# Kernel tuning notes

Measured on AMD Instinct MI355X. Metric: run time of the kernel, lower is better.

The kernel has to match this reference:

```python
import jax, jax.numpy as jnp
import numpy as np

N = 50000   # num_nodes
D = 128     # h_dim
R = 32      # num_rels * 2 (forward + inverse relations)
B = 8       # num_bases
E = 600000  # num_edges


def setup_inputs() -> dict:
    key = jax.random.key(0)
    ks = jax.random.split(key, 14)
    s = 1.0 / np.sqrt(D)
    return {
        "h_ids": jnp.arange(N, dtype=jnp.int32),
        "src": jax.random.randint(ks[0], (E,), 0, N),
        "dst": jax.random.randint(ks[1], (E,), 0, N),
        "etype": jax.random.randint(ks[2], (E,), 0, R),
        "norm": jax.random.uniform(ks[3], (E, 1), dtype=jnp.float32),
        "embedding": jax.random.normal(ks[4], (N, D), dtype=jnp.float32) * 0.05,
        "w_comp1": jax.random.normal(ks[5], (R, B), dtype=jnp.float32) * (1.0 / np.sqrt(B)),
        "bases1": jax.random.normal(ks[6], (B, D, D), dtype=jnp.float32) * s,
        "loop_w1": jax.random.normal(ks[7], (D, D), dtype=jnp.float32) * s,
        "bias1": jnp.zeros((D,), dtype=jnp.float32),
        "w_comp2": jax.random.normal(ks[8], (R, B), dtype=jnp.float32) * (1.0 / np.sqrt(B)),
        "bases2": jax.random.normal(ks[9], (B, D, D), dtype=jnp.float32) * s,
        "loop_w2": jax.random.normal(ks[10], (D, D), dtype=jnp.float32) * s,
        "bias2": jnp.zeros((D,), dtype=jnp.float32),
    }


def _rel_graph_conv(h, src, dst, etype, norm, w_comp, bases, loop_w, bias, act):
    # basis decomposition: W[r] = sum_b w_comp[r,b] * bases[b]
    W = jnp.einsum('rb,bio->rio', w_comp, bases)          # [R, D, D]
    # transform every node by every relation weight (dense GEMM)
    all_t = jnp.einsum('ni,rio->nro', h, W)               # [N, R, D]
    # per-edge gather of relation-specific transformed source features
    msg = all_t[src, etype] * norm                        # [E, D]
    # scatter-aggregate messages at destination nodes
    agg = jax.ops.segment_sum(msg, dst, num_segments=h.shape[0])  # [N, D]
    out = agg + h @ loop_w + bias                         # self-loop + bias
    return act(out) if act is not None else out


def reference(h_ids, src, dst, etype, norm, embedding,
              w_comp1, bases1, loop_w1, bias1,
              w_comp2, bases2, loop_w2, bias2):
    # EmbeddingLayer
    h = embedding[h_ids]                                  # [N, D]
    # hidden layer 0: relu activation (idx < num_hidden_layers-1)
    h = _rel_graph_conv(h, src, dst, etype, norm, w_comp1, bases1, loop_w1, bias1, jax.nn.relu)
    # hidden layer 1: no activation (last layer)
    h = _rel_graph_conv(h, src, dst, etype, norm, w_comp2, bases2, loop_w2, bias2, None)
    return h
```

## Files before the change

### kernel.cpp

```cpp
#include <hip/hip_runtime.h>

#define DD 128
#define NB 8
#define KTOT 1152

typedef unsigned int uint_t;
typedef __attribute__((ext_vector_type(8))) _Float16 half8v;
typedef __attribute__((ext_vector_type(2))) _Float16 half2v;
typedef __attribute__((ext_vector_type(4))) float f32x4;

static __device__ __forceinline__ void gld_lds16(const _Float16* g, _Float16* l)
{
  __builtin_amdgcn_global_load_lds(
      (const __attribute__((address_space(1))) void*)g,
      (__attribute__((address_space(3))) void*)l, 16, 0, 0);
}

static __device__ __forceinline__ half2v bc_h2(uint_t u)
{
  union { uint_t u; half2v h; } c; c.u = u; return c.h;
}

static __device__ __forceinline__ float fdot2(uint_t a, uint_t b, float acc)
{
#if __has_builtin(__builtin_amdgcn_fdot2)
  return __builtin_amdgcn_fdot2(bc_h2(a), bc_h2(b), acc, false);
#else
  half2v x = bc_h2(a), y = bc_h2(b);
  return acc + (float)x[0] * (float)y[0] + (float)x[1] * (float)y[1];
#endif
}

__global__ __launch_bounds__(256) void k_prep_w(
    const float* __restrict__ bases1, const float* __restrict__ loopw1,
    const float* __restrict__ bases2, const float* __restrict__ loopw2,
    _Float16* __restrict__ WcA)
{
  int i = blockIdx.x * 256 + threadIdx.x;
  if (i >= 2 * 36 * DD * 32) return;
  int layer = i / (36 * DD * 32);
  int rem   = i % (36 * DD * 32);
  int ks    = rem / (DD * 32);
  int rem2  = rem % (DD * 32);
  int feat  = rem2 / 32;
  int j     = rem2 % 32;
  int k     = ks * 32 + j;
  const float* basesL = layer ? bases2 : bases1;
  const float* loopwL = layer ? loopw2 : loopw1;
  float v;
  if (k < 1024) {
    int kk = k >> 3, b = k & 7;
    v = basesL[((size_t)b * DD + kk) * DD + feat];
  } else {
    v = loopwL[(size_t)(k - 1024) * DD + feat];
  }
  WcA[i] = (_Float16)v;
}

__global__ __launch_bounds__(256) void k_cast(
    const float* __restrict__ h, const int* __restrict__ ids,
    _Float16* __restrict__ hf, int N)
{
  int i = blockIdx.x * 256 + threadIdx.x;
  if (i >= N * (DD / 8)) return;
  int n  = i / (DD / 8);
  int k8 = (i % (DD / 8)) * 8;
  int row = ids ? ids[n] : n;
  const float* hp = h + (size_t)row * DD + k8;
  float4 v0 = *(const float4*)hp;
  float4 v1 = *(const float4*)(hp + 4);
  union { _Float16 e[8]; uint4 q; } p;
  p.e[0]=(_Float16)v0.x; p.e[1]=(_Float16)v0.y; p.e[2]=(_Float16)v0.z; p.e[3]=(_Float16)v0.w;
  p.e[4]=(_Float16)v1.x; p.e[5]=(_Float16)v1.y; p.e[6]=(_Float16)v1.z; p.e[7]=(_Float16)v1.w;
  *(uint4*)&hf[(size_t)n * DD + k8] = p.q;
}

__global__ __launch_bounds__(256) void k_zero(int* __restrict__ p, int n)
{
  int i = blockIdx.x * 256 + threadIdx.x;
  if (i < n) p[i] = 0;
}

__global__ __launch_bounds__(256) void k_hist(
    const int* __restrict__ dst, int* __restrict__ cnt,
    int* __restrict__ slotin, int E)
{
  int e = blockIdx.x * 256 + threadIdx.x;
  if (e < E) slotin[e] = atomicAdd(&cnt[dst[e]], 1);
}

__global__ __launch_bounds__(256) void k_bsum(
    const int* __restrict__ cnt, int* __restrict__ bsum, int N)
{
  __shared__ int s[256];
  int i = blockIdx.x * 256 + threadIdx.x;
  s[threadIdx.x] = (i < N) ? ((cnt[i] + 1) & ~1) : 0;
  __syncthreads();
  for (int off = 128; off > 0; off >>= 1) {
    if (threadIdx.x < off) s[threadIdx.x] += s[threadIdx.x + off];
    __syncthreads();
  }
  if (threadIdx.x == 0) bsum[blockIdx.x] = s[0];
}

__global__ __launch_bounds__(256) void k_scanb(
    const int* __restrict__ bsum, int* __restrict__ boff, int nb)
{
  __shared__ int s[256];
  int t = threadIdx.x;
  int own = (t < nb) ? bsum[t] : 0;
  s[t] = own;
  __syncthreads();
  for (int off = 1; off < 256; off <<= 1) {
    int v = (t >= off) ? s[t - off] : 0;
    __syncthreads();
    s[t] += v;
    __syncthreads();
  }
  if (t < nb) boff[t] = s[t] - own;
}

__global__ __launch_bounds__(256) void k_scan3(
    const int* __restrict__ cnt, const int* __restrict__ boff,
    int* __restrict__ row_start, int* __restrict__ psrc, int N)
{
  __shared__ int s[256];
  int t = threadIdx.x;
  int i = blockIdx.x * 256 + t;
  int c = (i < N) ? cnt[i] : 0;
  int v = (c + 1) & ~1;
  s[t] = v;
  __syncthreads();
  for (int off = 1; off < 256; off <<= 1) {
    int u = (t >= off) ? s[t - off] : 0;
    __syncthreads();
    s[t] += u;
    __syncthreads();
  }
  if (i < N) {
    int rs = boff[blockIdx.x] + s[t] - v;
    row_start[i] = rs;
    if (c & 1) psrc[rs + c] = 0;
  }
}

__global__ __launch_bounds__(256) void k_place(
    const int* __restrict__ dst, const int* __restrict__ src,
    const int* __restrict__ etype, const float* __restrict__ norm,
    const int* __restrict__ row_start, const int* __restrict__ slotin,
    int* __restrict__ psrc, int2* __restrict__ en, int E)
{
  int e = blockIdx.x * 256 + threadIdx.x;
  if (e < E) {
    int slot = row_start[dst[e]] + slotin[e];
    psrc[slot] = src[e];
    en[slot] = make_int2(etype[e], __float_as_int(norm[e]));
  }
}

__global__ __launch_bounds__(256) void k_payload_pair(
    const int2* __restrict__ en,
    const float* __restrict__ wcomp1, const float* __restrict__ wcomp2,
    _Float16* __restrict__ c1, _Float16* __restrict__ c2, int npair)
{
  int i = blockIdx.x * 256 + threadIdx.x;
  if (i >= npair) return;
  int2 e0 = en[2 * i], e1 = en[2 * i + 1];
  float n0 = __int_as_float(e0.y), n1 = __int_as_float(e1.y);
  const float* w10 = wcomp1 + e0.x * NB;
  const float* w11 = wcomp1 + e1.x * NB;
  const float* w20 = wcomp2 + e0.x * NB;
  const float* w21 = wcomp2 + e1.x * NB;

  union { _Float16 h[16]; uint4 q[2]; } p;
  #pragma unroll
  for (int b = 0; b < NB; b++) {
    p.h[b * 2]     = (_Float16)(w10[b] * n0);
    p.h[b * 2 + 1] = (_Float16)(w11[b] * n1);
  }
  *(uint4*)&c1[(size_t)i * 16]     = p.q[0];
  *(uint4*)&c1[(size_t)i * 16 + 8] = p.q[1];
  #pragma unroll
  for (int b = 0; b < NB; b++) {
    p.h[b * 2]     = (_Float16)(w20[b] * n0);
    p.h[b * 2 + 1] = (_Float16)(w21[b] * n1);
  }
  *(uint4*)&c2[(size_t)i * 16]     = p.q[0];
  *(uint4*)&c2[(size_t)i * 16 + 8] = p.q[1];
}

__global__ __launch_bounds__(256) void k_agg(
    const int* __restrict__ rowst, const int* __restrict__ cnt,
    const int* __restrict__ psrc, const _Float16* __restrict__ cpair,
    const _Float16* __restrict__ hf,
    _Float16* __restrict__ agg, int N)
{
  int v = blockIdx.x * 4 + (threadIdx.x >> 6);
  if (v >= N) return;
  int lane = threadIdx.x & 63;
  const uint_t* hf32 = (const uint_t*)hf;
  const int beg = rowst[v];
  const int npairs = (cnt[v] + 1) >> 1;
  const uint_t* cp = (const uint_t*)cpair + (size_t)(beg >> 1) * 8;
  const int* ps = psrc + beg;

  float ax[NB] = {}, ay[NB] = {};
  int i = 0;
  for (; i + 4 <= npairs; i += 4) {
    uint_t u[8], lo[4], hi[4];
    #pragma unroll
    for (int q = 0; q < 8; q++)
      u[q] = hf32[(size_t)ps[2*i + q] * 64 + lane];
    #pragma unroll
    for (int q = 0; q < 4; q++) {
      lo[q] = __builtin_amdgcn_perm(u[2*q], u[2*q+1], 0x01000504);
      hi[q] = __builtin_amdgcn_perm(u[2*q], u[2*q+1], 0x03020706);
    }
    #pragma unroll
    for (int b = 0; b < NB; b++) {
      #pragma unroll
      for (int q = 0; q < 4; q++) {
        uint_t cc = cp[(size_t)(i + q) * 8 + b];
        ax[b] = fdot2(cc, lo[q], ax[b]);
        ay[b] = fdot2(cc, hi[q], ay[b]);
      }
    }
  }
  for (; i + 2 <= npairs; i += 2) {
    uint_t u0 = hf32[(size_t)ps[2*i + 0] * 64 + lane];
    uint_t u1 = hf32[(size_t)ps[2*i + 1] * 64 + lane];
    uint_t u2 = hf32[(size_t)ps[2*i + 2] * 64 + lane];
    uint_t u3 = hf32[(size_t)ps[2*i + 3] * 64 + lane];
    uint_t lo01 = __builtin_amdgcn_perm(u0, u1, 0x01000504);
    uint_t hi01 = __builtin_amdgcn_perm(u0, u1, 0x03020706);
    uint_t lo23 = __builtin_amdgcn_perm(u2, u3, 0x01000504);
    uint_t hi23 = __builtin_amdgcn_perm(u2, u3, 0x03020706);
    #pragma unroll
    for (int b = 0; b < NB; b++) {
      uint_t ca = cp[(size_t)i * 8 + b];
      uint_t cb = cp[(size_t)(i + 1) * 8 + b];
      ax[b] = fdot2(ca, lo01, ax[b]);
      ay[b] = fdot2(ca, hi01, ay[b]);
      ax[b] = fdot2(cb, lo23, ax[b]);
      ay[b] = fdot2(cb, hi23, ay[b]);
    }
  }
  if (i < npairs) {
    uint_t u0 = hf32[(size_t)ps[2*i + 0] * 64 + lane];
    uint_t u1 = hf32[(size_t)ps[2*i + 1] * 64 + lane];
    uint_t lo01 = __builtin_amdgcn_perm(u0, u1, 0x01000504);
    uint_t hi01 = __builtin_amdgcn_perm(u0, u1, 0x03020706);
    #pragma unroll
    for (int b = 0; b < NB; b++) {
      uint_t ca = cp[(size_t)i * 8 + b];
      ax[b] = fdot2(ca, lo01, ax[b]);
      ay[b] = fdot2(ca, hi01, ay[b]);
    }
  }

  union { _Float16 e[8]; uint4 q; } p0, p1;
  #pragma unroll
  for (int b = 0; b < NB; b++) { p0.e[b] = (_Float16)ax[b]; p1.e[b] = (_Float16)ay[b]; }
  uint4* dstp = (uint4*)&agg[(size_t)v * 1024 + lane * 16];
  dstp[0] = p0.q;
  dstp[1] = p1.q;
}

template <int LAYER>
__global__ __launch_bounds__(256) void k_mm(
    const _Float16* __restrict__ agg,
    const _Float16* __restrict__ hf,
    const _Float16* __restrict__ WcA,
    const float* __restrict__ bias,
    float* __restrict__ outf, _Float16* __restrict__ outh, int N)
{
  __shared__ _Float16 sB[2][4096];

  const int n0   = blockIdx.x * 64;
  const int wv   = threadIdx.x >> 6;
  const int lane = threadIdx.x & 63;
  const int l15  = lane & 15, l4 = lane >> 4;

  int nodeL = n0 + lane; if (nodeL >= N) nodeL = N - 1;

  f32x4 acc[2][4];
  #pragma unroll
  for (int a = 0; a < 2; a++)
    #pragma unroll
    for (int b = 0; b < 4; b++) acc[a][b] = (f32x4)0.f;

  const int fbase = wv * 32 + l15;
  const int koff  = l4 * 8;

  auto STAGE = [&](int buf, int t) {
    const _Float16 *g0, *g1;
    if (t < 16) {
      g0 = &agg[(size_t)nodeL * 1024 + (2 * t)     * 32 + wv * 8];
      g1 = &agg[(size_t)nodeL * 1024 + (2 * t + 1) * 32 + wv * 8];
    } else {
      g0 = &hf[(size_t)nodeL * DD + (2 * t - 32) * 32 + wv * 8];
      g1 = &hf[(size_t)nodeL * DD + (2 * t - 31) * 32 + wv * 8];
    }
    gld_lds16(g0, &sB[buf][ wv      * 512]);
    gld_lds16(g1, &sB[buf][(wv + 4) * 512]);
  };

  auto COMPUTE = [&](int buf, int t) {
    #pragma unroll
    for (int sub = 0; sub < 2; sub++) {
      const int ks = 2 * t + sub;
      half8v af[2], bfr[4];
      #pragma unroll
      for (int mf = 0; mf < 2; mf++)
        af[mf] = *(const half8v*)&WcA[((size_t)ks * DD + fbase + mf * 16) * 32 + koff];
      #pragma unroll
      for (int nf = 0; nf < 4; nf++)
        bfr[nf] = *(const half8v*)&sB[buf][(l4 + sub * 4) * 512 + (nf * 16 + l15) * 8];
      #pragma unroll
      for (int mf = 0; mf < 2; mf++)
        #pragma unroll
        for (int nf = 0; nf < 4; nf++)
          acc[mf][nf] = __builtin_amdgcn_mfma_f32_16x16x32_f16(af[mf], bfr[nf], acc[mf][nf], 0, 0, 0);
    }
  };

  STAGE(0, 0);
  __syncthreads();
  int cur = 0;
  for (int t = 0; t < 17; t++) {
    STAGE(cur ^ 1, t + 1);
    COMPUTE(cur, t);
    __syncthreads();
    cur ^= 1;
  }
  COMPUTE(cur, 17);

  #pragma unroll
  for (int mf = 0; mf < 2; mf++)
    #pragma unroll
    for (int nf = 0; nf < 4; nf++) {
      int n = n0 + nf * 16 + l15;
      if (n >= N) continue;
      int feat = wv * 32 + mf * 16 + l4 * 4;
      if (LAYER == 1) {
        union { _Float16 e[4]; uint2 q; } p;
        #pragma unroll
        for (int r = 0; r < 4; r++)
          p.e[r] = (_Float16)fmaxf(acc[mf][nf][r] + bias[feat + r], 0.f);
        *(uint2*)&outh[(size_t)n * DD + feat] = p.q;
      } else {
        float4 o;
        o.x = acc[mf][nf][0] + bias[feat + 0];
        o.y = acc[mf][nf][1] + bias[feat + 1];
        o.z = acc[mf][nf][2] + bias[feat + 2];
        o.w = acc[mf][nf][3] + bias[feat + 3];
        *(float4*)&outf[(size_t)n * DD + feat] = o;
      }
    }
}

extern "C" void kernel_launch(void* const* d_in, const int* in_sizes, int n_in,
                              void* d_out, int out_size, void* d_ws, size_t ws_size,
                              hipStream_t stream)
{
  const int*   h_ids     = (const int*)d_in[0];
  const int*   src       = (const int*)d_in[1];
  const int*   dst       = (const int*)d_in[2];
  const int*   etype     = (const int*)d_in[3];
  const float* norm      = (const float*)d_in[4];
  const float* embedding = (const float*)d_in[5];
  const float* w_comp1   = (const float*)d_in[6];
  const float* bases1    = (const float*)d_in[7];
  const float* loop_w1   = (const float*)d_in[8];
  const float* bias1     = (const float*)d_in[9];
  const float* w_comp2   = (const float*)d_in[10];
  const float* bases2    = (const float*)d_in[11];
  const float* loop_w2   = (const float*)d_in[12];
  const float* bias2     = (const float*)d_in[13];

  const int N = in_sizes[0];
  const int E = in_sizes[1];
  const int S = (E + N) & ~1;
  const int NPAIR = S >> 1;
  const int NBLK = (N + 255) / 256;

  char* base = (char*)d_ws;
  size_t off = 0;
  auto alloc = [&](size_t bytes) -> char* {
    char* p = base + off;
    off += (bytes + 255) & ~(size_t)255;
    return p;
  };
  _Float16* agg  = (_Float16*)alloc((size_t)N * 1024 * 2);
  _Float16* hfp  = (_Float16*)alloc((size_t)N * DD * 2);
  _Float16* h1h  = (_Float16*)alloc((size_t)N * DD * 2);
  _Float16* WcA  = (_Float16*)alloc((size_t)2 * 36 * DD * 32 * 2);
  int*      cnt    = (int*)   alloc((size_t)N * 4);
  int2*     en     = (int2*)  alloc((size_t)S * 8);
  int*      rowst  = (int*)   alloc((size_t)N * 4);
  int*      bsum   = (int*)   alloc(256 * 4);
  int*      boff   = (int*)   alloc(256 * 4);
  int*      slotin = (int*)   alloc((size_t)E * 4);
  int*      psrc   = (int*)   alloc((size_t)S * 4);
  _Float16* c1     = (_Float16*)alloc((size_t)S * 8 * 2);
  _Float16* c2     = (_Float16*)alloc((size_t)S * 8 * 2);
  float*    out    = (float*)d_out;

  int zn = (int)(((char*)(en + S) - (char*)cnt) / 4);
  k_zero <<<(zn + 255) / 256, 256, 0, stream>>>(cnt, zn);
  k_hist <<<(E + 255) / 256, 256, 0, stream>>>(dst, cnt, slotin, E);
  k_bsum <<<NBLK, 256, 0, stream>>>(cnt, bsum, N);
  k_scanb<<<1, 256, 0, stream>>>(bsum, boff, NBLK);
  k_scan3<<<NBLK, 256, 0, stream>>>(cnt, boff, rowst, psrc, N);
  k_place<<<(E + 255) / 256, 256, 0, stream>>>(dst, src, etype, norm,
                                               rowst, slotin, psrc, en, E);
  k_payload_pair<<<(NPAIR + 255) / 256, 256, 0, stream>>>(
      en, w_comp1, w_comp2, c1, c2, NPAIR);

  k_prep_w<<<(2 * 36 * DD * 32 + 255) / 256, 256, 0, stream>>>(bases1, loop_w1, bases2, loop_w2, WcA);

  dim3 gmm((N + 63) / 64);
  int gagg = (N + 3) / 4;

  k_cast<<<(N * (DD / 8) + 255) / 256, 256, 0, stream>>>(embedding, h_ids, hfp, N);
  k_agg<<<gagg, 256, 0, stream>>>(rowst, cnt, psrc, c1, hfp, agg, N);
  k_mm<1><<<gmm, 256, 0, stream>>>(agg, hfp, WcA, bias1, nullptr, h1h, N);

  k_agg<<<gagg, 256, 0, stream>>>(rowst, cnt, psrc, c2, h1h, agg, N);
  k_mm<2><<<gmm, 256, 0, stream>>>(agg, h1h, WcA + (size_t)36 * DD * 32, bias2, out, nullptr, N);
}
```

Measured before the change: 255.7 us.

## Split k_mm across 8 waves and pack edge records into int4

The GEMM kernel now runs 512 threads per block. Each of the 8 waves owns 16 output features instead of 32, which halves the accumulators and A-fragment loads per wave, and staging issues one LDS load per wave instead of two. The edge placement step writes a single int4 record holding src, etype and norm, and the payload kernel writes psrc from it. This removes the separate psrc scatter and the odd-count padding write in the scan. Odd-count padding slots rely on the zeroed en4 buffer to yield src 0, and the wider record adds scatter bytes.

```diff
diff --git a/kernel.cpp b/kernel.cpp
--- a/kernel.cpp
+++ b/kernel.cpp
@@ -122,7 +122,7 @@
 
 __global__ __launch_bounds__(256) void k_scan3(
     const int* __restrict__ cnt, const int* __restrict__ boff,
-    int* __restrict__ row_start, int* __restrict__ psrc, int N)
+    int* __restrict__ row_start, int N)
 {
   __shared__ int s[256];
   int t = threadIdx.x;
@@ -137,53 +137,50 @@
     s[t] += u;
     __syncthreads();
   }
-  if (i < N) {
-    int rs = boff[blockIdx.x] + s[t] - v;
-    row_start[i] = rs;
-    if (c & 1) psrc[rs + c] = 0;
-  }
+  if (i < N) row_start[i] = boff[blockIdx.x] + s[t] - v;
 }
 
 __global__ __launch_bounds__(256) void k_place(
     const int* __restrict__ dst, const int* __restrict__ src,
     const int* __restrict__ etype, const float* __restrict__ norm,
     const int* __restrict__ row_start, const int* __restrict__ slotin,
-    int* __restrict__ psrc, int2* __restrict__ en, int E)
+    int4* __restrict__ en4, int E)
 {
   int e = blockIdx.x * 256 + threadIdx.x;
   if (e < E) {
     int slot = row_start[dst[e]] + slotin[e];
-    psrc[slot] = src[e];
-    en[slot] = make_int2(etype[e], __float_as_int(norm[e]));
+    en4[slot] = make_int4(src[e], etype[e], __float_as_int(norm[e]), 0);
   }
 }
 
 __global__ __launch_bounds__(256) void k_payload_pair(
-    const int2* __restrict__ en,
+    const int4* __restrict__ en4,
     const float* __restrict__ wcomp1, const float* __restrict__ wcomp2,
+    int* __restrict__ psrc,
     _Float16* __restrict__ c1, _Float16* __restrict__ c2, int npair)
 {
   int i = blockIdx.x * 256 + threadIdx.x;
   if (i >= npair) return;
-  int2 e0 = en[2 * i], e1 = en[2 * i + 1];
-  float n0 = __int_as_float(e0.y), n1 = __int_as_float(e1.y);
-  const float* w10 = wcomp1 + e0.x * NB;
-  const float* w11 = wcomp1 + e1.x * NB;
-  const float* w20 = wcomp2 + e0.x * NB;
-  const float* w21 = wcomp2 + e1.x * NB;
+  int4 a = en4[2 * i], b = en4[2 * i + 1];
+  float n0 = __int_as_float(a.z), n1 = __int_as_float(b.z);
+  *(int2*)&psrc[2 * i] = make_int2(a.x, b.x);
+  const float* w10 = wcomp1 + a.y * NB;
+  const float* w11 = wcomp1 + b.y * NB;
+  const float* w20 = wcomp2 + a.y * NB;
+  const float* w21 = wcomp2 + b.y * NB;
 
   union { _Float16 h[16]; uint4 q[2]; } p;
   #pragma unroll
-  for (int b = 0; b < NB; b++) {
-    p.h[b * 2]     = (_Float16)(w10[b] * n0);
-    p.h[b * 2 + 1] = (_Float16)(w11[b] * n1);
+  for (int bb = 0; bb < NB; bb++) {
+    p.h[bb * 2]     = (_Float16)(w10[bb] * n0);
+    p.h[bb * 2 + 1] = (_Float16)(w11[bb] * n1);
   }
   *(uint4*)&c1[(size_t)i * 16]     = p.q[0];
   *(uint4*)&c1[(size_t)i * 16 + 8] = p.q[1];
   #pragma unroll
-  for (int b = 0; b < NB; b++) {
-    p.h[b * 2]     = (_Float16)(w20[b] * n0);
-    p.h[b * 2 + 1] = (_Float16)(w21[b] * n1);
+  for (int bb = 0; bb < NB; bb++) {
+    p.h[bb * 2]     = (_Float16)(w20[bb] * n0);
+    p.h[bb * 2 + 1] = (_Float16)(w21[bb] * n1);
   }
   *(uint4*)&c2[(size_t)i * 16]     = p.q[0];
   *(uint4*)&c2[(size_t)i * 16 + 8] = p.q[1];
@@ -267,7 +264,7 @@
 }
 
 template <int LAYER>
-__global__ __launch_bounds__(256) void k_mm(
+__global__ __launch_bounds__(512) void k_mm(
     const _Float16* __restrict__ agg,
     const _Float16* __restrict__ hf,
     const _Float16* __restrict__ WcA,
@@ -283,44 +280,32 @@
 
   int nodeL = n0 + lane; if (nodeL >= N) nodeL = N - 1;
 
-  f32x4 acc[2][4];
+  f32x4 acc[4];
   #pragma unroll
-  for (int a = 0; a < 2; a++)
-    #pragma unroll
-    for (int b = 0; b < 4; b++) acc[a][b] = (f32x4)0.f;
-
-  const int fbase = wv * 32 + l15;
+  for (int b = 0; b < 4; b++) acc[b] = (f32x4)0.f;
+
+  const int fbase = wv * 16 + l15;
   const int koff  = l4 * 8;
 
   auto STAGE = [&](int buf, int t) {
-    const _Float16 *g0, *g1;
-    if (t < 16) {
-      g0 = &agg[(size_t)nodeL * 1024 + (2 * t)     * 32 + wv * 8];
-      g1 = &agg[(size_t)nodeL * 1024 + (2 * t + 1) * 32 + wv * 8];
-    } else {
-      g0 = &hf[(size_t)nodeL * DD + (2 * t - 32) * 32 + wv * 8];
-      g1 = &hf[(size_t)nodeL * DD + (2 * t - 31) * 32 + wv * 8];
-    }
-    gld_lds16(g0, &sB[buf][ wv      * 512]);
-    gld_lds16(g1, &sB[buf][(wv + 4) * 512]);
+    const _Float16* g;
+    if (t < 16) g = &agg[(size_t)nodeL * 1024 + t * 64 + wv * 8];
+    else        g = &hf [(size_t)nodeL * DD   + (t - 16) * 64 + wv * 8];
+    gld_lds16(g, &sB[buf][wv * 512]);
   };
 
   auto COMPUTE = [&](int buf, int t) {
     #pragma unroll
     for (int sub = 0; sub < 2; sub++) {
       const int ks = 2 * t + sub;
-      half8v af[2], bfr[4];
-      #pragma unroll
-      for (int mf = 0; mf < 2; mf++)
-        af[mf] = *(const half8v*)&WcA[((size_t)ks * DD + fbase + mf * 16) * 32 + koff];
+      half8v af = *(const half8v*)&WcA[((size_t)ks * DD + fbase) * 32 + koff];
+      half8v bfr[4];
       #pragma unroll
       for (int nf = 0; nf < 4; nf++)
-        bfr[nf] = *(const half8v*)&sB[buf][(l4 + sub * 4) * 512 + (nf * 16 + l15) * 8];
+        bfr[nf] = *(const half8v*)&sB[buf][(sub * 4 + l4) * 512 + (nf * 16 + l15) * 8];
       #pragma unroll
-      for (int mf = 0; mf < 2; mf++)
-        #pragma unroll
-        for (int nf = 0; nf < 4; nf++)
-          acc[mf][nf] = __builtin_amdgcn_mfma_f32_16x16x32_f16(af[mf], bfr[nf], acc[mf][nf], 0, 0, 0);
+      for (int nf = 0; nf < 4; nf++)
+        acc[nf] = __builtin_amdgcn_mfma_f32_16x16x32_f16(af, bfr[nf], acc[nf], 0, 0, 0);
     }
   };
 
@@ -336,27 +321,25 @@
   COMPUTE(cur, 17);
 
   #pragma unroll
-  for (int mf = 0; mf < 2; mf++)
-    #pragma unroll
-    for (int nf = 0; nf < 4; nf++) {
-      int n = n0 + nf * 16 + l15;
-      if (n >= N) continue;
-      int feat = wv * 32 + mf * 16 + l4 * 4;
-      if (LAYER == 1) {
-        union { _Float16 e[4]; uint2 q; } p;
-        #pragma unroll
-        for (int r = 0; r < 4; r++)
-          p.e[r] = (_Float16)fmaxf(acc[mf][nf][r] + bias[feat + r], 0.f);
-        *(uint2*)&outh[(size_t)n * DD + feat] = p.q;
-      } else {
-        float4 o;
-        o.x = acc[mf][nf][0] + bias[feat + 0];
-        o.y = acc[mf][nf][1] + bias[feat + 1];
-        o.z = acc[mf][nf][2] + bias[feat + 2];
-        o.w = acc[mf][nf][3] + bias[feat + 3];
-        *(float4*)&outf[(size_t)n * DD + feat] = o;
-      }
-    }
+  for (int nf = 0; nf < 4; nf++) {
+    int n = n0 + nf * 16 + l15;
+    if (n >= N) continue;
+    int feat = wv * 16 + l4 * 4;
+    if (LAYER == 1) {
+      union { _Float16 e[4]; uint2 q; } p;
+      #pragma unroll
+      for (int r = 0; r < 4; r++)
+        p.e[r] = (_Float16)fmaxf(acc[nf][r] + bias[feat + r], 0.f);
+      *(uint2*)&outh[(size_t)n * DD + feat] = p.q;
+    } else {
+      float4 o;
+      o.x = acc[nf][0] + bias[feat + 0];
+      o.y = acc[nf][1] + bias[feat + 1];
+      o.z = acc[nf][2] + bias[feat + 2];
+      o.w = acc[nf][3] + bias[feat + 3];
+      *(float4*)&outf[(size_t)n * DD + feat] = o;
+    }
+  }
 }
 
 extern "C" void kernel_launch(void* const* d_in, const int* in_sizes, int n_in,
@@ -396,7 +379,7 @@
   _Float16* h1h  = (_Float16*)alloc((size_t)N * DD * 2);
   _Float16* WcA  = (_Float16*)alloc((size_t)2 * 36 * DD * 32 * 2);
   int*      cnt    = (int*)   alloc((size_t)N * 4);
-  int2*     en     = (int2*)  alloc((size_t)S * 8);
+  int4*     en4    = (int4*)  alloc((size_t)S * 16);
   int*      rowst  = (int*)   alloc((size_t)N * 4);
   int*      bsum   = (int*)   alloc(256 * 4);
   int*      boff   = (int*)   alloc(256 * 4);
@@ -406,16 +389,16 @@
   _Float16* c2     = (_Float16*)alloc((size_t)S * 8 * 2);
   float*    out    = (float*)d_out;
 
-  int zn = (int)(((char*)(en + S) - (char*)cnt) / 4);
+  int zn = (int)(((char*)(en4 + S) - (char*)cnt) / 4);
   k_zero <<<(zn + 255) / 256, 256, 0, stream>>>(cnt, zn);
   k_hist <<<(E + 255) / 256, 256, 0, stream>>>(dst, cnt, slotin, E);
   k_bsum <<<NBLK, 256, 0, stream>>>(cnt, bsum, N);
   k_scanb<<<1, 256, 0, stream>>>(bsum, boff, NBLK);
-  k_scan3<<<NBLK, 256, 0, stream>>>(cnt, boff, rowst, psrc, N);
+  k_scan3<<<NBLK, 256, 0, stream>>>(cnt, boff, rowst, N);
   k_place<<<(E + 255) / 256, 256, 0, stream>>>(dst, src, etype, norm,
-                                               rowst, slotin, psrc, en, E);
+                                               rowst, slotin, en4, E);
   k_payload_pair<<<(NPAIR + 255) / 256, 256, 0, stream>>>(
-      en, w_comp1, w_comp2, c1, c2, NPAIR);
+      en4, w_comp1, w_comp2, psrc, c1, c2, NPAIR);
 
   k_prep_w<<<(2 * 36 * DD * 32 + 255) / 256, 256, 0, stream>>>(bases1, loop_w1, bases2, loop_w2, WcA);
 
@@ -424,8 +407,8 @@
 
   k_cast<<<(N * (DD / 8) + 255) / 256, 256, 0, stream>>>(embedding, h_ids, hfp, N);
   k_agg<<<gagg, 256, 0, stream>>>(rowst, cnt, psrc, c1, hfp, agg, N);
-  k_mm<1><<<gmm, 256, 0, stream>>>(agg, hfp, WcA, bias1, nullptr, h1h, N);
+  k_mm<1><<<gmm, 512, 0, stream>>>(agg, hfp, WcA, bias1, nullptr, h1h, N);
 
   k_agg<<<gagg, 256, 0, stream>>>(rowst, cnt, psrc, c2, h1h, agg, N);
-  k_mm<2><<<gmm, 256, 0, stream>>>(agg, h1h, WcA + (size_t)36 * DD * 32, bias2, out, nullptr, N);
-}
+  k_mm<2><<<gmm, 512, 0, stream>>>(agg, h1h, WcA + (size_t)36 * DD * 32, bias2, out, nullptr, N);
+}
```

New measurement: 244.7 us. 1.05x faster.
